# Optimization experiments

Hardware: AMD Instinct MI355X
Metric: run time of the kernel (lower is better)

## Reference

```python
import jax, jax.numpy as jnp
import numpy as np

N, K = 262144, 8
IN_F, H_F, OUT_F = 16, 128, 16
NEG_SLOPE = 0.01  # torch LeakyReLU default


def setup_inputs() -> dict:
    key = jax.random.key(0)
    ks = jax.random.split(key, 10)
    h = jax.random.normal(ks[0], (N, IN_F), dtype=jnp.float32)
    pos = jax.random.uniform(ks[1], (N, 3), dtype=jnp.float32)
    nbr_idx = jax.random.randint(ks[2], (N, K), 0, N)

    def xavier(k, shape):
        fan_in, fan_out = shape[0], shape[1]
        a = jnp.sqrt(6.0 / (fan_in + fan_out))
        return jax.random.uniform(k, shape, jnp.float32, -a, a)

    W0 = xavier(ks[3], (K * IN_F, H_F))
    b0 = xavier(ks[4], (1, H_F))
    W1 = xavier(ks[5], (K * H_F, H_F))
    b1 = xavier(ks[6], (1, H_F))
    W2 = xavier(ks[7], (K * H_F, OUT_F))
    b2 = xavier(ks[8], (1, OUT_F))
    return {"h": h, "pos": pos, "nbr_idx": nbr_idx,
            "W0": W0, "b0": b0, "W1": W1, "b1": b1, "W2": W2, "b2": b2}


def _layer(h, pos, nbr_idx, W, b, activation):
    # gather neighbor messages and positions: [N, K, F], [N, K, 3]
    msgs = h[nbr_idx]
    src_pos = pos[nbr_idx]
    diff = pos[:, None, :] - src_pos                       # [N, K, 3]
    dist = jnp.sqrt(jnp.sum(diff * diff, axis=2, keepdims=True))  # [N, K, 1]
    dist = jnp.where(dist == 0, jnp.float32(0.5), dist)
    wow = (msgs / dist).reshape(h.shape[0], -1)            # [N, K*F]
    out = wow @ W + b
    if activation:
        out = jnp.where(out >= 0, out, NEG_SLOPE * out)
    return out


def reference(h, pos, nbr_idx, W0, b0, W1, b1, W2, b2):
    h1 = _layer(h, pos, nbr_idx, W0, b0, False)   # input layer
    h2 = _layer(h1, pos, nbr_idx, W1, b1, True)   # hidden layer (LeakyReLU)
    h3 = _layer(h2, pos, nbr_idx, W2, b2, False)  # output layer
    return h3
```

## Files before the change

### kernel.cpp

```cpp
#include <hip/hip_runtime.h>
#include <hip/hip_fp16.h>


typedef _Float16 f16x8 __attribute__((ext_vector_type(8)));
typedef float f32x4 __attribute__((ext_vector_type(4)));

#define NNODES 262144

__global__ __launch_bounds__(256) void conv_h_kernel(const float* __restrict__ h,
                                                     __half* __restrict__ h16, int n) {
    int i = blockIdx.x * 256 + threadIdx.x;
    if (i < n) h16[i] = __float2half(h[i]);
}

__global__ __launch_bounds__(256) void prep_edges_kernel(const float* __restrict__ pos,
                                                         const int* __restrict__ nbr,
                                                         __half* __restrict__ invd, int n_edges) {
    int e = blockIdx.x * 256 + threadIdx.x;
    if (e >= n_edges) return;
    int i = e >> 3;
    int n = nbr[e];
    float dx = pos[i * 3 + 0] - pos[n * 3 + 0];
    float dy = pos[i * 3 + 1] - pos[n * 3 + 1];
    float dz = pos[i * 3 + 2] - pos[n * 3 + 2];
    float d = sqrtf(dx * dx + dy * dy + dz * dz);
    if (d == 0.0f) d = 0.5f;
    invd[e] = __float2half((1.0f / d) * 0.00390625f);
}

__global__ __launch_bounds__(256) void shuffle_w_kernel(const float* __restrict__ W,
                                                        __half* __restrict__ Wf,
                                                        int KT, int FO) {
    int e = blockIdx.x * 256 + threadIdx.x;
    if (e >= KT * FO) return;
    int j = e & 7;
    int lane = (e >> 3) & 63;
    int rest = e >> 9;
    int NT = FO >> 4;
    int t = rest % NT;
    int s = rest / NT;
    int k = s * 32 + (lane >> 4) * 8 + j;
    int n = t * 16 + (lane & 15);
    Wf[e] = __float2half(W[k * FO + n]);
}

__global__ __launch_bounds__(256) void shuffle_w2s_kernel(const float* __restrict__ W2,
                                                          __half* __restrict__ Wf) {
    int e = blockIdx.x * 256 + threadIdx.x;
    if (e >= 128 * 128) return;
    int j = e & 7;
    int lane = (e >> 3) & 63;
    int rest = e >> 9;
    int t = rest % 8;
    int s = rest / 8;
    int k = s * 32 + (lane >> 4) * 8 + j;
    Wf[e] = __float2half(W2[(size_t)(t * 128 + k) * 16 + (lane & 15)]);
}

__global__ __launch_bounds__(256) void layer0_kernel(
    const __half* __restrict__ hprev, const __half* __restrict__ invd,
    const int* __restrict__ nbr, const __half* __restrict__ Wf,
    const float* __restrict__ bias, __half* __restrict__ outp) {
    __shared__ __align__(16) __half Bs[16384];

    const int tid = threadIdx.x;
    const int wave = tid >> 6;
    const int lane = tid & 63;
    const int quad = lane >> 4;
    const int lmod = lane & 15;
    const int mbase = blockIdx.x * 128 + wave * 16 + lmod;

    int idx[2][8];
    f16x8 invr[2];
#pragma unroll
    for (int mt = 0; mt < 2; ++mt) {
        const int m = mbase + mt * 64;
        const int4* nrow = (const int4*)(nbr + (size_t)m * 8);
        const int4 iA = nrow[0];
        const int4 iB = nrow[1];
        idx[mt][0] = iA.x; idx[mt][1] = iA.y; idx[mt][2] = iA.z; idx[mt][3] = iA.w;
        idx[mt][4] = iB.x; idx[mt][5] = iB.y; idx[mt][6] = iB.z; idx[mt][7] = iB.w;
        invr[mt] = *(const f16x8*)(invd + (size_t)m * 8);
    }

    f32x4 acc[2][8];
#pragma unroll
    for (int mt = 0; mt < 2; ++mt)
#pragma unroll
        for (int t = 0; t < 8; ++t) acc[mt][t] = f32x4{0.f, 0.f, 0.f, 0.f};

    {
        const uint4* src = (const uint4*)Wf;
        uint4* dst = (uint4*)Bs;
#pragma unroll
        for (int i = 0; i < 8; ++i) dst[i * 256 + tid] = src[i * 256 + tid];
    }
    __syncthreads();

#pragma unroll
    for (int s = 0; s < 4; ++s) {
        const int nb = 2 * s + (quad >> 1);
        f16x8 as[2];
#pragma unroll
        for (int mt = 0; mt < 2; ++mt) {
            f16x8 av = *(const f16x8*)(hprev + (size_t)idx[mt][nb] * 16 + (quad & 1) * 8);
            as[mt] = av * invr[mt][nb];
        }
#pragma unroll
        for (int t = 0; t < 8; ++t) {
            f16x8 b = *(const f16x8*)(Bs + ((size_t)(s * 8 + t) * 64 + lane) * 8);
#pragma unroll
            for (int mt = 0; mt < 2; ++mt)
                acc[mt][t] = __builtin_amdgcn_mfma_f32_16x16x32_f16(as[mt], b, acc[mt][t], 0, 0, 0);
        }
    }

#pragma unroll
    for (int mt = 0; mt < 2; ++mt) {
        const int rbase = blockIdx.x * 128 + mt * 64 + wave * 16 + quad * 4;
#pragma unroll
        for (int t = 0; t < 8; ++t) {
            const int col = t * 16 + lmod;
            const float bv = bias[col];
#pragma unroll
            for (int rr = 0; rr < 4; ++rr) {
                float v = acc[mt][t][rr] * 256.0f + bv;
                outp[(size_t)(rbase + rr) * 128 + col] = __float2half(v);
            }
        }
    }
}

__device__ __forceinline__ int off16(int seg, int row) {
    return seg * 64 + (row & ~15) + ((row ^ seg) & 15);
}

__global__ __launch_bounds__(256, 3) void layer1p_kernel(
    const __half* __restrict__ hprev, const __half* __restrict__ invd,
    const int* __restrict__ nbr, const __half* __restrict__ Wf,
    const __half* __restrict__ Wf2s, const float* __restrict__ bias,
    __half* __restrict__ Pout) {
    __shared__ __align__(16) __half As[2][8192];

    const int tid = threadIdx.x;
    const int wave = tid >> 6;
    const int lane = tid & 63;
    const int quad = lane >> 4;
    const int lmod = lane & 15;
    const int rowblk = blockIdx.x * 64;
    const int seg = lmod;

    int srow[4], grow_[4], soff[4];
#pragma unroll
    for (int i = 0; i < 4; ++i) {
        srow[i] = wave * 16 + i * 4 + quad;
        grow_[i] = rowblk + srow[i];
        soff[i] = off16(seg, srow[i]) * 8;
    }

    f16x8 invS[4];
#pragma unroll
    for (int i = 0; i < 4; ++i) invS[i] = *(const f16x8*)(invd + (size_t)grow_[i] * 8);

    int idxA[4], idxB[4], idxR[2][4];
#pragma unroll
    for (int i = 0; i < 4; ++i) {
        idxA[i] = nbr[(size_t)grow_[i] * 8 + 0];
        idxB[i] = nbr[(size_t)grow_[i] * 8 + 1];
        idxR[0][i] = nbr[(size_t)grow_[i] * 8 + 2];
        idxR[1][i] = nbr[(size_t)grow_[i] * 8 + 3];
    }

    const __half* WfB = Wf + ((size_t)(wave * 2) * 64 + lane) * 8;

    f16x8 Bc[4][2], Bn[4][2];
#pragma unroll
    for (int ks = 0; ks < 4; ++ks)
#pragma unroll
        for (int tl = 0; tl < 2; ++tl)
            Bc[ks][tl] = *(const f16x8*)(WfB + (size_t)(ks * 8 + tl) * 512);

    int roff[4][4];
#pragma unroll
    for (int m = 0; m < 4; ++m)
#pragma unroll
        for (int ks = 0; ks < 4; ++ks)
            roff[m][ks] = off16(ks * 4 + quad, m * 16 + lmod) * 8;

    f16x8 ga[2][4];
#pragma unroll
    for (int i = 0; i < 4; ++i)
        ga[0][i] = *(const f16x8*)(hprev + (size_t)idxA[i] * 128 + seg * 8);
#pragma unroll
    for (int i = 0; i < 4; ++i)
        ga[1][i] = *(const f16x8*)(hprev + (size_t)idxB[i] * 128 + seg * 8);

#pragma unroll
    for (int i = 0; i < 4; ++i) {
        f16x8 v = ga[0][i] * invS[i][0];
        *(f16x8*)(&As[0][soff[i]]) = v;
    }
    __syncthreads();

    f32x4 acc[4][2];
#pragma unroll
    for (int m = 0; m < 4; ++m) { acc[m][0] = f32x4{0.f,0.f,0.f,0.f}; acc[m][1] = f32x4{0.f,0.f,0.f,0.f}; }

#pragma unroll
    for (int nb = 0; nb < 8; ++nb) {
        const int cur = nb & 1;
        if (nb < 6) {
#pragma unroll
            for (int i = 0; i < 4; ++i)
                ga[cur][i] = *(const f16x8*)(hprev + (size_t)idxR[cur][i] * 128 + seg * 8);
        }
        if (nb < 4) {
#pragma unroll
            for (int i = 0; i < 4; ++i)
                idxR[cur][i] = nbr[(size_t)grow_[i] * 8 + nb + 4];
        }
        if (nb < 7) {
#pragma unroll
            for (int ks = 0; ks < 4; ++ks)
#pragma unroll
                for (int tl = 0; tl < 2; ++tl)
                    Bn[ks][tl] = *(const f16x8*)(WfB + (size_t)(((nb + 1) * 4 + ks) * 8 + tl) * 512);
        }
#pragma unroll
        for (int m = 0; m < 4; ++m) {
#pragma unroll
            for (int ks = 0; ks < 4; ++ks) {
                f16x8 a = *(const f16x8*)(&As[cur][roff[m][ks]]);
                acc[m][0] = __builtin_amdgcn_mfma_f32_16x16x32_f16(a, Bc[ks][0], acc[m][0], 0, 0, 0);
                acc[m][1] = __builtin_amdgcn_mfma_f32_16x16x32_f16(a, Bc[ks][1], acc[m][1], 0, 0, 0);
            }
        }
        if (nb < 7) {
#pragma unroll
            for (int i = 0; i < 4; ++i) {
                f16x8 v = ga[(nb + 1) & 1][i] * invS[i][nb + 1];
                *(f16x8*)(&As[cur ^ 1][soff[i]]) = v;
            }
#pragma unroll
            for (int ks = 0; ks < 4; ++ks) { Bc[ks][0] = Bn[ks][0]; Bc[ks][1] = Bn[ks][1]; }
            __syncthreads();
        }
    }

    __half* As0 = &As[0][0];
#pragma unroll
    for (int m = 0; m < 4; ++m) {
#pragma unroll
        for (int tl = 0; tl < 2; ++tl) {
            const int col = wave * 32 + tl * 16 + lmod;
            const float bv = bias[col];
            const int sg = col >> 3;
            const int jj = col & 7;
#pragma unroll
            for (int rr = 0; rr < 4; ++rr) {
                const int row = m * 16 + quad * 4 + rr;
                float v = acc[m][tl][rr] * 256.0f + bv;
                v = (v >= 0.f) ? v : 0.01f * v;
                As0[off16(sg, row) * 8 + jj] = __float2half(v);
            }
        }
    }
    __syncthreads();

    const __half* WfB2 = Wf2s + ((size_t)(wave * 2) * 64 + lane) * 8;
    f16x8 B2[4][2];
#pragma unroll
    for (int ks = 0; ks < 4; ++ks)
#pragma unroll
        for (int tl = 0; tl < 2; ++tl)
            B2[ks][tl] = *(const f16x8*)(WfB2 + (size_t)(ks * 8 + tl) * 512);

    f32x4 acc2[4][2];
#pragma unroll
    for (int m = 0; m < 4; ++m) { acc2[m][0] = f32x4{0.f,0.f,0.f,0.f}; acc2[m][1] = f32x4{0.f,0.f,0.f,0.f}; }
#pragma unroll
    for (int m = 0; m < 4; ++m) {
#pragma unroll
        for (int ks = 0; ks < 4; ++ks) {
            f16x8 a2 = *(const f16x8*)(&As0[roff[m][ks]]);
            acc2[m][0] = __builtin_amdgcn_mfma_f32_16x16x32_f16(a2, B2[ks][0], acc2[m][0], 0, 0, 0);
            acc2[m][1] = __builtin_amdgcn_mfma_f32_16x16x32_f16(a2, B2[ks][1], acc2[m][1], 0, 0, 0);
        }
    }

#pragma unroll
    for (int m = 0; m < 4; ++m) {
#pragma unroll
        for (int tl = 0; tl < 2; ++tl) {
            const int col = wave * 32 + tl * 16 + lmod;
#pragma unroll
            for (int rr = 0; rr < 4; ++rr) {
                const int grow = rowblk + m * 16 + quad * 4 + rr;
                Pout[(size_t)grow * 128 + col] = __float2half(acc2[m][tl][rr]);
            }
        }
    }
}

__global__ __launch_bounds__(256) void reduce_kernel(
    const __half* __restrict__ P, const __half* __restrict__ invd,
    const int* __restrict__ nbr, const float* __restrict__ b2,
    float* __restrict__ outp) {
    const int d = blockIdx.x * 256 + threadIdx.x;

    const int4* nrow = (const int4*)(nbr + (size_t)d * 8);
    const int4 iA = nrow[0];
    const int4 iB = nrow[1];
    const int idx[8] = {iA.x, iA.y, iA.z, iA.w, iB.x, iB.y, iB.z, iB.w};
    const f16x8 iv = *(const f16x8*)(invd + (size_t)d * 8);

    f16x8 lo[8], hi[8];
#pragma unroll
    for (int k = 0; k < 8; ++k) {
        const __half* p = P + (size_t)idx[k] * 128 + k * 16;
        lo[k] = *(const f16x8*)p;
        hi[k] = *(const f16x8*)(p + 8);
    }

    float acc[16];
#pragma unroll
    for (int c = 0; c < 16; ++c) acc[c] = 0.f;
#pragma unroll
    for (int k = 0; k < 8; ++k) {
        const float w = (float)iv[k];
#pragma unroll
        for (int c = 0; c < 8; ++c) {
            acc[c] += w * (float)lo[k][c];
            acc[c + 8] += w * (float)hi[k][c];
        }
    }

    float4 o[4];
#pragma unroll
    for (int q = 0; q < 4; ++q) {
        o[q].x = acc[q * 4 + 0] * 256.0f + b2[q * 4 + 0];
        o[q].y = acc[q * 4 + 1] * 256.0f + b2[q * 4 + 1];
        o[q].z = acc[q * 4 + 2] * 256.0f + b2[q * 4 + 2];
        o[q].w = acc[q * 4 + 3] * 256.0f + b2[q * 4 + 3];
    }
    float4* dst = (float4*)(outp + (size_t)d * 16);
#pragma unroll
    for (int q = 0; q < 4; ++q) dst[q] = o[q];
}

extern "C" void kernel_launch(void* const* d_in, const int* in_sizes, int n_in,
                              void* d_out, int out_size, void* d_ws, size_t ws_size,
                              hipStream_t stream) {
    const float* h   = (const float*)d_in[0];
    const float* pos = (const float*)d_in[1];
    const int*   nbr = (const int*)d_in[2];
    const float* W0  = (const float*)d_in[3];
    const float* b0  = (const float*)d_in[4];
    const float* W1  = (const float*)d_in[5];
    const float* b1  = (const float*)d_in[6];
    const float* W2  = (const float*)d_in[7];
    const float* b2  = (const float*)d_in[8];

    const int N = NNODES;

    char* w = (char*)d_ws;
    __half* h1 = (__half*)w;
    __half* P  = (__half*)(w + (size_t)67108864);
    __half* invd2 = (__half*)w;

    char* ob = (char*)d_out;
    __half* invd = (__half*)(ob + 0);
    __half* h16  = (__half*)(ob + 4194304);
    __half* W0f  = (__half*)(ob + 12582912);
    __half* W1f  = (__half*)(ob + 12615680);
    __half* Wf2s = (__half*)(ob + 12877824);

    conv_h_kernel<<<(N * 16 + 255) / 256, 256, 0, stream>>>(h, h16, N * 16);
    prep_edges_kernel<<<(N * 8 + 255) / 256, 256, 0, stream>>>(pos, nbr, invd, N * 8);
    shuffle_w_kernel<<<(128 * 128 + 255) / 256, 256, 0, stream>>>(W0, W0f, 128, 128);
    shuffle_w_kernel<<<(1024 * 128 + 255) / 256, 256, 0, stream>>>(W1, W1f, 1024, 128);
    shuffle_w2s_kernel<<<(128 * 128 + 255) / 256, 256, 0, stream>>>(W2, Wf2s);

    layer0_kernel<<<N / 128, 256, 0, stream>>>(h16, invd, nbr, W0f, b0, h1);
    layer1p_kernel<<<N / 64, 256, 0, stream>>>(h1, invd, nbr, W1f, Wf2s, b1, P);

    (void)hipMemcpyAsync(invd2, invd, 4194304, hipMemcpyDeviceToDevice, stream);

    reduce_kernel<<<N / 256, 256, 0, stream>>>(P, invd2, nbr, b2, (float*)d_out);
}
```

Before: 317.8 us.

## Gather neighbor rows directly into LDS and apply inverse distance after load

Replaces the register-staged neighbor gather with direct global-to-LDS loads, using a swizzled row mapping so each lane's write lands in the bank-conflict-free layout. Inverse-distance scaling moves from the staging store to the LDS-read side, just before each MFMA. Weight register buffers are halved by streaming B in half-steps, which allows raising launch bounds from 3 to 4 blocks per CU. The aim is to cut register pressure and VGPR round-trips on the gather and raise occupancy to hide gather latency, at the cost of extra multiplies per MFMA operand.

```diff
diff --git a/kernel.cpp b/kernel.cpp
--- a/kernel.cpp
+++ b/kernel.cpp
@@ -6,6 +6,12 @@
 typedef float f32x4 __attribute__((ext_vector_type(4)));
 
 #define NNODES 262144
+
+__device__ __forceinline__ void gload_lds16(const __half* g, __half* l) {
+    __builtin_amdgcn_global_load_lds(
+        (const __attribute__((address_space(1))) unsigned int*)g,
+        (__attribute__((address_space(3))) unsigned int*)l, 16, 0, 0);
+}
 
 __global__ __launch_bounds__(256) void conv_h_kernel(const float* __restrict__ h,
                                                      __half* __restrict__ h16, int n) {
@@ -135,7 +141,7 @@
     return seg * 64 + (row & ~15) + ((row ^ seg) & 15);
 }
 
-__global__ __launch_bounds__(256, 3) void layer1p_kernel(
+__global__ __launch_bounds__(256, 4) void layer1p_kernel(
     const __half* __restrict__ hprev, const __half* __restrict__ invd,
     const int* __restrict__ nbr, const __half* __restrict__ Wf,
     const __half* __restrict__ Wf2s, const float* __restrict__ bias,
@@ -148,103 +154,99 @@
     const int quad = lane >> 4;
     const int lmod = lane & 15;
     const int rowblk = blockIdx.x * 64;
-    const int seg = lmod;
-
-    int srow[4], grow_[4], soff[4];
+
+    int grow2[4];
 #pragma unroll
     for (int i = 0; i < 4; ++i) {
-        srow[i] = wave * 16 + i * 4 + quad;
-        grow_[i] = rowblk + srow[i];
-        soff[i] = off16(seg, srow[i]) * 8;
-    }
-
-    f16x8 invS[4];
-#pragma unroll
-    for (int i = 0; i < 4; ++i) invS[i] = *(const f16x8*)(invd + (size_t)grow_[i] * 8);
+        const int row = (lane & 48) | ((lane & 15) ^ (wave * 4 + i));
+        grow2[i] = rowblk + row;
+    }
 
     int idxA[4], idxB[4], idxR[2][4];
 #pragma unroll
     for (int i = 0; i < 4; ++i) {
-        idxA[i] = nbr[(size_t)grow_[i] * 8 + 0];
-        idxB[i] = nbr[(size_t)grow_[i] * 8 + 1];
-        idxR[0][i] = nbr[(size_t)grow_[i] * 8 + 2];
-        idxR[1][i] = nbr[(size_t)grow_[i] * 8 + 3];
+        const int* nb_ = nbr + (size_t)grow2[i] * 8;
+        idxA[i] = nb_[0];
+        idxB[i] = nb_[1];
+        idxR[0][i] = nb_[2];
+    }
+
+    f16x8 invF[4];
+#pragma unroll
+    for (int m = 0; m < 4; ++m)
+        invF[m] = *(const f16x8*)(invd + (size_t)(rowblk + m * 16 + lmod) * 8);
+
+    int roff4[4];
+#pragma unroll
+    for (int ks = 0; ks < 4; ++ks) {
+        const int seg = ks * 4 + quad;
+        roff4[ks] = (seg * 64 + ((lmod ^ seg) & 15)) * 8;
     }
 
     const __half* WfB = Wf + ((size_t)(wave * 2) * 64 + lane) * 8;
 
-    f16x8 Bc[4][2], Bn[4][2];
-#pragma unroll
-    for (int ks = 0; ks < 4; ++ks)
+    f16x8 Bc[2][2], Bn[2][2];
+#pragma unroll
+    for (int ks2 = 0; ks2 < 2; ++ks2)
 #pragma unroll
         for (int tl = 0; tl < 2; ++tl)
-            Bc[ks][tl] = *(const f16x8*)(WfB + (size_t)(ks * 8 + tl) * 512);
-
-    int roff[4][4];
-#pragma unroll
-    for (int m = 0; m < 4; ++m)
-#pragma unroll
-        for (int ks = 0; ks < 4; ++ks)
-            roff[m][ks] = off16(ks * 4 + quad, m * 16 + lmod) * 8;
-
-    f16x8 ga[2][4];
+            Bc[ks2][tl] = *(const f16x8*)(WfB + (size_t)(ks2 * 8 + tl) * 512);
+
 #pragma unroll
     for (int i = 0; i < 4; ++i)
-        ga[0][i] = *(const f16x8*)(hprev + (size_t)idxA[i] * 128 + seg * 8);
-#pragma unroll
-    for (int i = 0; i < 4; ++i)
-        ga[1][i] = *(const f16x8*)(hprev + (size_t)idxB[i] * 128 + seg * 8);
-
-#pragma unroll
-    for (int i = 0; i < 4; ++i) {
-        f16x8 v = ga[0][i] * invS[i][0];
-        *(f16x8*)(&As[0][soff[i]]) = v;
-    }
+        gload_lds16(hprev + (size_t)idxA[i] * 128 + (wave * 4 + i) * 8,
+                    &As[0][(size_t)(wave * 256 + i * 64) * 8]);
+
+    f32x4 acc[4][2];
+#pragma unroll
+    for (int m = 0; m < 4; ++m) { acc[m][0] = f32x4{0.f,0.f,0.f,0.f}; acc[m][1] = f32x4{0.f,0.f,0.f,0.f}; }
+
     __syncthreads();
-
-    f32x4 acc[4][2];
-#pragma unroll
-    for (int m = 0; m < 4; ++m) { acc[m][0] = f32x4{0.f,0.f,0.f,0.f}; acc[m][1] = f32x4{0.f,0.f,0.f,0.f}; }
 
 #pragma unroll
     for (int nb = 0; nb < 8; ++nb) {
         const int cur = nb & 1;
-        if (nb < 6) {
+        if (nb < 7) {
+#pragma unroll
+            for (int i = 0; i < 4; ++i) {
+                const int id = (nb == 0) ? idxB[i] : idxR[(nb + 1) & 1][i];
+                gload_lds16(hprev + (size_t)id * 128 + (wave * 4 + i) * 8,
+                            &As[cur ^ 1][(size_t)(wave * 256 + i * 64) * 8]);
+            }
+        }
+        if (nb < 5) {
 #pragma unroll
             for (int i = 0; i < 4; ++i)
-                ga[cur][i] = *(const f16x8*)(hprev + (size_t)idxR[cur][i] * 128 + seg * 8);
-        }
-        if (nb < 4) {
-#pragma unroll
-            for (int i = 0; i < 4; ++i)
-                idxR[cur][i] = nbr[(size_t)grow_[i] * 8 + nb + 4];
-        }
-        if (nb < 7) {
-#pragma unroll
-            for (int ks = 0; ks < 4; ++ks)
-#pragma unroll
-                for (int tl = 0; tl < 2; ++tl)
-                    Bn[ks][tl] = *(const f16x8*)(WfB + (size_t)(((nb + 1) * 4 + ks) * 8 + tl) * 512);
-        }
-#pragma unroll
-        for (int m = 0; m < 4; ++m) {
-#pragma unroll
-            for (int ks = 0; ks < 4; ++ks) {
-                f16x8 a = *(const f16x8*)(&As[cur][roff[m][ks]]);
-                acc[m][0] = __builtin_amdgcn_mfma_f32_16x16x32_f16(a, Bc[ks][0], acc[m][0], 0, 0, 0);
-                acc[m][1] = __builtin_amdgcn_mfma_f32_16x16x32_f16(a, Bc[ks][1], acc[m][1], 0, 0, 0);
-            }
-        }
-        if (nb < 7) {
-#pragma unroll
-            for (int i = 0; i < 4; ++i) {
-                f16x8 v = ga[(nb + 1) & 1][i] * invS[i][nb + 1];
-                *(f16x8*)(&As[cur ^ 1][soff[i]]) = v;
-            }
-#pragma unroll
-            for (int ks = 0; ks < 4; ++ks) { Bc[ks][0] = Bn[ks][0]; Bc[ks][1] = Bn[ks][1]; }
-            __syncthreads();
-        }
+                idxR[(nb + 1) & 1][i] = nbr[(size_t)grow2[i] * 8 + nb + 3];
+        }
+#pragma unroll
+        for (int h = 0; h < 2; ++h) {
+            const int p = nb * 2 + h;
+            if (p < 15) {
+#pragma unroll
+                for (int ks2 = 0; ks2 < 2; ++ks2)
+#pragma unroll
+                    for (int tl = 0; tl < 2; ++tl)
+                        Bn[ks2][tl] = *(const f16x8*)(WfB + (size_t)(((p + 1) * 2 + ks2) * 8 + tl) * 512);
+            }
+#pragma unroll
+            for (int m = 0; m < 4; ++m) {
+#pragma unroll
+                for (int ks2 = 0; ks2 < 2; ++ks2) {
+                    const int ks = h * 2 + ks2;
+                    f16x8 a = *(const f16x8*)(&As[cur][roff4[ks] + m * 128]);
+                    a = a * invF[m][nb];
+                    acc[m][0] = __builtin_amdgcn_mfma_f32_16x16x32_f16(a, Bc[ks2][0], acc[m][0], 0, 0, 0);
+                    acc[m][1] = __builtin_amdgcn_mfma_f32_16x16x32_f16(a, Bc[ks2][1], acc[m][1], 0, 0, 0);
+                }
+            }
+#pragma unroll
+            for (int ks2 = 0; ks2 < 2; ++ks2) {
+                Bc[ks2][0] = Bn[ks2][0];
+                Bc[ks2][1] = Bn[ks2][1];
+            }
+        }
+        if (nb < 7) __syncthreads();
     }
 
     __half* As0 = &As[0][0];
@@ -282,7 +284,7 @@
     for (int m = 0; m < 4; ++m) {
 #pragma unroll
         for (int ks = 0; ks < 4; ++ks) {
-            f16x8 a2 = *(const f16x8*)(&As0[roff[m][ks]]);
+            f16x8 a2 = *(const f16x8*)(&As0[roff4[ks] + m * 128]);
             acc2[m][0] = __builtin_amdgcn_mfma_f32_16x16x32_f16(a2, B2[ks][0], acc2[m][0], 0, 0, 0);
             acc2[m][1] = __builtin_amdgcn_mfma_f32_16x16x32_f16(a2, B2[ks][1], acc2[m][1], 0, 0, 0);
         }
```

After: 355.2 us. 1.12x slower.
